# Kernel tuning notes

Hardware: AMD Instinct MI355X
Metric: run time of the kernel (lower is better)

The kernel has to match this reference:

```python
import jax, jax.numpy as jnp
import numpy as np

H = 8
D = 512
DK = D // H  # 64
ALPHA = 0.2  # leaky relu negative slope


def setup_inputs() -> dict:
    key = jax.random.key(0)
    ks = jax.random.split(key, 10)
    B, N = 8, 1024
    query = jax.random.normal(ks[0], (B, N, D), dtype=jnp.float32)
    key_t = jax.random.normal(ks[1], (B, N, D), dtype=jnp.float32)
    value = jax.random.normal(ks[2], (B, N, D), dtype=jnp.float32)
    mask = jax.random.randint(ks[3], (B, N, N), 0, 2, dtype=jnp.int32)
    scale = 0.02
    Wq = jax.random.normal(ks[4], (D, D), dtype=jnp.float32) * scale
    Wk = jax.random.normal(ks[5], (D, D), dtype=jnp.float32) * scale
    Wv = jax.random.normal(ks[6], (D, D), dtype=jnp.float32) * scale
    Wo = jax.random.normal(ks[7], (D, D), dtype=jnp.float32) * scale
    bq = jnp.zeros((D,), jnp.float32)
    bk = jnp.zeros((D,), jnp.float32)
    bv = jnp.zeros((D,), jnp.float32)
    bo = jnp.zeros((D,), jnp.float32)
    # xavier-uniform-like init for the attention vector a: shape (h, 2*d_k)
    limit = float(np.sqrt(6.0 / (H + 2 * DK)))
    a = jax.random.uniform(ks[8], (H, 2 * DK), dtype=jnp.float32, minval=-limit, maxval=limit)
    return {"query": query, "key": key_t, "value": value, "mask": mask,
            "Wq": Wq, "bq": bq, "Wk": Wk, "bk": bk, "Wv": Wv, "bv": bv,
            "Wo": Wo, "bo": bo, "a": a}


def reference(query, key, value, mask, Wq, bq, Wk, bk, Wv, bv, Wo, bo, a):
    B, N, _ = query.shape

    def proj(x, W, b):
        # torch Linear: x @ W.T + b, then split heads -> (B, H, N, DK)
        return (x @ W.T + b).reshape(B, N, H, DK).transpose(0, 2, 1, 3)

    q = proj(query, Wq, bq)
    k = proj(key, Wk, bk)
    v = proj(value, Wv, bv)

    # 'cat' attention: scores[b,h,i,j] = concat(q_i, k_j) . a[h]
    #                = q_i . a[h,:DK] + k_j . a[h,DK:]  (algebraic decomposition,
    #                 avoids the O(N^2 * 2*DK) concat tensor of the torch code)
    sq = jnp.einsum('bhnd,hd->bhn', q, a[:, :DK])
    sk = jnp.einsum('bhnd,hd->bhn', k, a[:, DK:])
    scores = sq[:, :, :, None] + sk[:, :, None, :]  # (B, H, N, N)

    # mask == 0 -> -inf (mask broadcast over heads), applied BEFORE leaky relu
    scores = jnp.where(mask[:, None, :, :] == 0, -jnp.inf, scores)
    # leaky relu (leaky_relu(-inf) == -inf, preserved)
    scores = jnp.where(scores >= 0, scores, ALPHA * scores)

    p = jax.nn.softmax(scores, axis=-1)
    # fully-masked rows produce NaN -> replace with 0 (as in the torch code)
    p = jnp.where(jnp.isnan(p), jnp.zeros_like(p), p)

    x = jnp.einsum('bhnm,bhmd->bhnd', p, v)
    x = x.transpose(0, 2, 1, 3).reshape(B, N, D)
    return x @ Wo.T + bo
```

## Files before the change

### kernel.cpp

```cpp
#include <hip/hip_runtime.h>
#include <hip/hip_bf16.h>
#include <stdint.h>


typedef __attribute__((ext_vector_type(8))) short short8;
typedef __attribute__((ext_vector_type(4))) float f32x4;

#define LB __launch_bounds__(256)

union U8 { unsigned u[4]; short8 s; uint4 v; };
union U2 { unsigned u[2]; uint2 v; };

__device__ __forceinline__ unsigned short f2bf(float f) {
  unsigned int u = __float_as_uint(f);
  u += 0x7fffu + ((u >> 16) & 1u);
  return (unsigned short)(u >> 16);
}

__device__ __forceinline__ unsigned cvt_pk(float a, float b) {
  unsigned r;
  asm("v_cvt_pk_bf16_f32 %0, %1, %2" : "=v"(r) : "v"(a), "v"(b));
  return r;
}

__device__ __forceinline__ void async_cp16(const void* g, void* l) {
  __builtin_amdgcn_global_load_lds(
      (const __attribute__((address_space(1))) unsigned int*)g,
      (__attribute__((address_space(3))) unsigned int*)l, 16, 0, 0);
}

__global__ LB void prep_kernel(const float* __restrict__ Wq, const float* __restrict__ Wk,
                               const float* __restrict__ a, const float* __restrict__ bq,
                               const float* __restrict__ bk,
                               unsigned short* __restrict__ Bfrag, float* __restrict__ qkb,
                               const float* __restrict__ Wv, const float* __restrict__ Wo,
                               unsigned short* __restrict__ wv16,
                               unsigned short* __restrict__ wo16) {
  const int blk = blockIdx.x;
  if (blk < 512) {
    const float* src = blk < 256 ? Wv : Wo;
    unsigned short* dst = blk < 256 ? wv16 : wo16;
    const int idx = ((blk & 255) * 256 + threadIdx.x) * 4;
    const float4 v = *(const float4*)(src + idx);
    U2 pk;
    pk.u[0] = cvt_pk(v.x, v.y);
    pk.u[1] = cvt_pk(v.z, v.w);
    *(uint2*)(dst + idx) = pk.v;
    return;
  }
  const int t = (blk - 512) * 256 + threadIdx.x;
  const int d = t & 511, h = t >> 9;
  float aq = 0.f, ak = 0.f;
#pragma unroll 4
  for (int dk = 0; dk < 64; ++dk) {
    aq += Wq[(size_t)(h * 64 + dk) * 512 + d] * a[h * 128 + dk];
    ak += Wk[(size_t)(h * 64 + dk) * 512 + d] * a[h * 128 + 64 + dk];
  }
  const float L2E = 1.4426950408889634f;
  const int ks = d >> 5, lch = (d >> 3) & 3, tt = d & 7;
  Bfrag[((ks * 64 + (lch << 4) + h) << 3) + tt] = f2bf(aq * L2E);
  Bfrag[((ks * 64 + (lch << 4) + 8 + h) << 3) + tt] = f2bf(ak * L2E);
  if (d == 0) {
    float s1 = 0.f, s2 = 0.f;
    for (int dk = 0; dk < 64; ++dk) {
      s1 += bq[h * 64 + dk] * a[h * 128 + dk];
      s2 += bk[h * 64 + dk] * a[h * 128 + 64 + dk];
    }
    qkb[h] = s1 * L2E;
    qkb[8 + h] = s2 * L2E;
  }
}

__global__ LB void sqsk_kernel(const float* __restrict__ query, const float* __restrict__ key,
                               const unsigned short* __restrict__ Bfrag,
                               const float* __restrict__ qkb,
                               float* __restrict__ sq, float* __restrict__ sk) {
  __shared__ float comb[3 * 64 * 9];
  const int tid = threadIdx.x, wv = tid >> 6, l = tid & 63;
  const int m0 = blockIdx.x * 16;
  const int k0 = wv * 128;
  short8 bf[4];
#pragma unroll
  for (int ks = 0; ks < 4; ++ks)
    bf[ks] = *(const short8*)(Bfrag + (((wv * 4 + ks) * 64 + l) << 3));
  const float* qbase = query + (size_t)(m0 + (l & 15)) * 512 + k0 + ((l >> 4) << 3);
  const float* kbase = key + (size_t)(m0 + (l & 15)) * 512 + k0 + ((l >> 4) << 3);
  f32x4 cq = {}, ck = {};
#pragma unroll
  for (int ks = 0; ks < 4; ++ks) {
    const float4 q0 = *(const float4*)(qbase + ks * 32);
    const float4 q1 = *(const float4*)(qbase + ks * 32 + 4);
    const float4 k0v = *(const float4*)(kbase + ks * 32);
    const float4 k1v = *(const float4*)(kbase + ks * 32 + 4);
    U8 aq, ak;
    aq.u[0] = cvt_pk(q0.x, q0.y); aq.u[1] = cvt_pk(q0.z, q0.w);
    aq.u[2] = cvt_pk(q1.x, q1.y); aq.u[3] = cvt_pk(q1.z, q1.w);
    ak.u[0] = cvt_pk(k0v.x, k0v.y); ak.u[1] = cvt_pk(k0v.z, k0v.w);
    ak.u[2] = cvt_pk(k1v.x, k1v.y); ak.u[3] = cvt_pk(k1v.z, k1v.w);
    cq = __builtin_amdgcn_mfma_f32_16x16x32_bf16(aq.s, bf[ks], cq, 0, 0, 0);
    ck = __builtin_amdgcn_mfma_f32_16x16x32_bf16(ak.s, bf[ks], ck, 0, 0, 0);
  }
  if (wv) {
    float* p = comb + ((wv - 1) * 64 + l) * 9;
#pragma unroll
    for (int r = 0; r < 4; ++r) { p[r] = cq[r]; p[4 + r] = ck[r]; }
  }
  __syncthreads();
  if (wv == 0) {
#pragma unroll
    for (int j = 0; j < 3; ++j) {
      const float* p = comb + (j * 64 + l) * 9;
#pragma unroll
      for (int r = 0; r < 4; ++r) { cq[r] += p[r]; ck[r] += p[4 + r]; }
    }
    const int col = l & 15;
    const int mbase = m0 + ((l >> 4) << 2);
    const int b = mbase >> 10;
    const float bia = qkb[col];
    if (col < 8) {
      float* out = sq + ((size_t)b * 8 + col) * 1024;
#pragma unroll
      for (int r = 0; r < 4; ++r) out[(mbase + r) & 1023] = cq[r] + bia;
    } else {
      float* out = sk + ((size_t)b * 8 + (col - 8)) * 1024;
#pragma unroll
      for (int r = 0; r < 4; ++r) out[(mbase + r) & 1023] = ck[r] + bia;
    }
  }
}

__global__ LB void maskbits_kernel(const int* __restrict__ mask,
                                   unsigned int* __restrict__ bits) {
  const size_t idx = (size_t)blockIdx.x * 256 + threadIdx.x;
  const unsigned long long bl = __ballot(mask[idx] != 0);
  if ((threadIdx.x & 63) == 0) {
    bits[idx >> 5] = (unsigned int)bl;
    bits[(idx >> 5) + 1] = (unsigned int)(bl >> 32);
  }
}

template <int AB16, int BB16, int MODE>
__global__ LB void gemm_bt(const void* __restrict__ Ap,
                           const void* __restrict__ Bwp,
                           const float* __restrict__ bias, void* __restrict__ outp) {
  __shared__ unsigned short As[32 * 32];
  __shared__ unsigned short Bs[128 * 32];
  const int tid = threadIdx.x;
  const int w = tid >> 6, l = tid & 63;
  const int lr = l & 15, lc = l >> 4;
  const int bm = blockIdx.x >> 2, bn = blockIdx.x & 3;
  const int m0 = bm * 32, n0 = bn * 128;
  const int wr = (w & 1) * 16, wc = (w >> 1) * 64;
  const int rch = (lc ^ ((lr >> 1) & 3)) << 3;
  const int crow = l >> 2;
  const int sc = (l & 3) ^ ((l >> 3) & 3);
  const unsigned short* a16 = (const unsigned short*)Ap;
  const unsigned short* b16 = (const unsigned short*)Bwp;
  const float* b32 = (const float*)Bwp;
  const unsigned short* bsrc0 = nullptr; const unsigned short* bsrc1 = nullptr;
  if (BB16) {
    bsrc0 = b16 + (size_t)(n0 + (w << 4) + crow) * 512 + (sc << 3);
    bsrc1 = b16 + (size_t)(n0 + ((w + 4) << 4) + crow) * 512 + (sc << 3);
  }
  const unsigned short* asrc = nullptr;
  if (AB16)
    asrc = a16 + (size_t)(m0 + ((w >> 1) << 4) + crow) * 512 + (sc << 3);

  f32x4 acc[4] = {};
  for (int kt = 0; kt < 16; ++kt) {
    const int k0 = kt * 32;
    if (kt) __syncthreads();
    if (AB16) {
      if (!(w & 1)) async_cp16(asrc + k0, As + ((w >> 1) << 9));
    } else {
      if (tid < 128) {
        const int row = tid >> 2, gr = tid & 3;
        const int sch = (gr ^ ((row >> 1) & 3)) << 3;
        const float4* src = (const float4*)((const float*)Ap + (size_t)(m0 + row) * 512 + k0 + gr * 8);
        const float4 a0 = src[0], a1 = src[1];
        U8 t8;
        t8.u[0] = cvt_pk(a0.x, a0.y); t8.u[1] = cvt_pk(a0.z, a0.w);
        t8.u[2] = cvt_pk(a1.x, a1.y); t8.u[3] = cvt_pk(a1.z, a1.w);
        *(uint4*)(As + row * 32 + sch) = t8.v;
      }
    }
    if (BB16) {
      async_cp16(bsrc0 + k0, Bs + (w << 9));
      async_cp16(bsrc1 + k0, Bs + ((w + 4) << 9));
    } else {
#pragma unroll
      for (int it = 0; it < 2; ++it) {
        const int idx = it * 256 + tid;
        const int row = idx >> 2, gr = idx & 3;
        const int sch = (gr ^ ((row >> 1) & 3)) << 3;
        const float4* src = (const float4*)(b32 + (size_t)(n0 + row) * 512 + k0 + gr * 8);
        const float4 b0 = src[0], b1 = src[1];
        U8 t8;
        t8.u[0] = cvt_pk(b0.x, b0.y); t8.u[1] = cvt_pk(b0.z, b0.w);
        t8.u[2] = cvt_pk(b1.x, b1.y); t8.u[3] = cvt_pk(b1.z, b1.w);
        *(uint4*)(Bs + row * 32 + sch) = t8.v;
      }
    }
    __syncthreads();
    const short8 af = *(const short8*)(As + (wr + lr) * 32 + rch);
#pragma unroll
    for (int j = 0; j < 4; ++j) {
      const short8 bfr = *(const short8*)(Bs + (wc + j * 16 + lr) * 32 + rch);
      acc[j] = __builtin_amdgcn_mfma_f32_16x16x32_bf16(af, bfr, acc[j], 0, 0, 0);
    }
  }
#pragma unroll
  for (int j = 0; j < 4; ++j) {
    const int nn = n0 + wc + j * 16 + lr;
    const float bia = bias[nn];
    const int mm0 = m0 + wr + lc * 4;
    if (MODE == 0) {
      float* out = (float*)outp;
#pragma unroll
      for (int r = 0; r < 4; ++r)
        out[(size_t)(mm0 + r) * 512 + nn] = acc[j][r] + bia;
    } else {
      unsigned short* out = (unsigned short*)outp;
      const int b = mm0 >> 10, t0 = mm0 & 1023;
      const int h = nn >> 6, dk = nn & 63;
      U2 pk;
      pk.u[0] = cvt_pk(acc[j][0] + bia, acc[j][1] + bia);
      pk.u[1] = cvt_pk(acc[j][2] + bia, acc[j][3] + bia);
      *(uint2*)(out + (((size_t)((b * 8 + h) * 64 + dk)) << 10) + t0) = pk.v;
    }
  }
}

__global__ LB void attn_kernel(const float* __restrict__ sq, const float* __restrict__ sk,
                               const unsigned char* __restrict__ mbits,
                               const unsigned short* __restrict__ vt,
                               unsigned short* __restrict__ xb) {
  __shared__ char smem[20480];
  unsigned short* vts = (unsigned short*)smem;
  float* sks = (float*)(smem + 8192);
  char* mks = smem + 12288;
  const int tid = threadIdx.x;
  const int w = tid >> 6, l = tid & 63;
  const int lr = l & 15, lc = l >> 4;
  const int bid = blockIdx.x;
  const int bh = bid >> 4, iblk = bid & 15;
  const int b = bh >> 3, h = bh & 7;
  const int i0b = iblk * 64;
  const float* sqp = sq + (size_t)bh * 1024;
  const float* skp = sk + (size_t)bh * 1024;
  const unsigned short* vtp = vt + ((size_t)bh << 16);
  const unsigned char* mrow = mbits + ((size_t)b << 17);

  async_cp16(skp + (w << 8) + l * 4, sks + (w << 8));
#pragma unroll
  for (int m = 0; m < 2; ++m) {
    const int row = (w << 4) + (m << 3) + (l >> 3);
    const int c = (l & 7) ^ (row & 7);
    async_cp16(mrow + (size_t)(i0b + row) * 128 + (c << 4), mks + (w << 11) + (m << 10));
  }
  const int strow = (w << 4) + (l >> 2);
  const int stc = (l & 3) ^ ((strow >> 1) & 3);
  const unsigned short* srcw = vtp + strow * 1024 + (stc << 3);
  async_cp16(srcw, vts + (w << 9));

  const int rowl = (w << 4) + lr;
  const float sq1 = sqp[i0b + rowl];
  __syncthreads();

  f32x4 acc[4] = {};
  f32x4 accs = {};
  short8 ones;
#pragma unroll
  for (int t = 0; t < 8; ++t) ones[t] = (short)0x3f80;
  const int mrowbase = rowl << 7;
  const int rxorb = (rowl & 7) << 4;
  const int vread = (lc ^ ((lr >> 1) & 3)) << 3;

  int cur = 0;
  for (int jt = 0; jt < 32; ++jt) {
    if (jt < 31) {
      async_cp16(srcw + (jt + 1) * 32, vts + ((cur ^ 1) << 11) + (w << 9));
      asm volatile("s_waitcnt vmcnt(1)" ::: "memory");
    } else {
      asm volatile("s_waitcnt vmcnt(0)" ::: "memory");
    }
    __builtin_amdgcn_sched_barrier(0);
    __builtin_amdgcn_s_barrier();
    const int jb = jt << 5;
    const unsigned int mb = (unsigned char)mks[mrowbase + ((jt * 4 + lc) ^ rxorb)];
    const f32x4 s0 = *(const f32x4*)(sks + jb + (lc << 3));
    const f32x4 s1 = *(const f32x4*)(sks + jb + (lc << 3) + 4);
    float e[8];
#pragma unroll
    for (int t = 0; t < 8; ++t) {
      float s = sq1 + (t < 4 ? s0[t] : s1[t - 4]);
      s = fmaxf(s, 0.2f * s);
      const float ex = __builtin_amdgcn_exp2f(s);
      e[t] = (mb & (1u << t)) ? ex : 0.0f;
    }
    U8 pa;
    pa.u[0] = cvt_pk(e[0], e[1]); pa.u[1] = cvt_pk(e[2], e[3]);
    pa.u[2] = cvt_pk(e[4], e[5]); pa.u[3] = cvt_pk(e[6], e[7]);
    const unsigned short* vb_base = vts + (cur << 11) + vread;
#pragma unroll
    for (int c = 0; c < 4; ++c) {
      const short8 bv = *(const short8*)(vb_base + ((c << 4) + lr) * 32);
      acc[c] = __builtin_amdgcn_mfma_f32_16x16x32_bf16(pa.s, bv, acc[c], 0, 0, 0);
    }
    accs = __builtin_amdgcn_mfma_f32_16x16x32_bf16(pa.s, ones, accs, 0, 0, 0);
    if (jt < 31) __builtin_amdgcn_s_barrier();
    cur ^= 1;
  }

#pragma unroll
  for (int r = 0; r < 4; ++r) {
    const float s = accs[r];
    const float inv = s > 0.0f ? 1.0f / s : 0.0f;
    const int i = i0b + (w << 4) + lc * 4 + r;
#pragma unroll
    for (int c = 0; c < 4; ++c)
      xb[(((size_t)(b * 1024 + i)) << 9) + h * 64 + c * 16 + lr] =
          f2bf(acc[c][r] * inv);
  }
}

extern "C" void kernel_launch(void* const* d_in, const int* in_sizes, int n_in,
                              void* d_out, int out_size, void* d_ws, size_t ws_size,
                              hipStream_t stream) {
  const float* query = (const float*)d_in[0];
  const float* key   = (const float*)d_in[1];
  const float* value = (const float*)d_in[2];
  const int*   mask  = (const int*)d_in[3];
  const float* Wq = (const float*)d_in[4];
  const float* bq = (const float*)d_in[5];
  const float* Wk = (const float*)d_in[6];
  const float* bk = (const float*)d_in[7];
  const float* Wv = (const float*)d_in[8];
  const float* bv = (const float*)d_in[9];
  const float* Wo = (const float*)d_in[10];
  const float* bo = (const float*)d_in[11];
  const float* a  = (const float*)d_in[12];

  char* oc = (char*)d_out;
  unsigned short* vt = (unsigned short*)(oc + 0);
  unsigned int* mbits = (unsigned int*)(oc + 8388608);
  float* sqv = (float*)(oc + 9437184);
  float* skv = (float*)(oc + 9699328);
  unsigned short* Bfrag = (unsigned short*)(oc + 9961472);
  float* qkb = (float*)(oc + 9977856);
  unsigned short* wv16 = (unsigned short*)(oc + 10485760);
  unsigned short* wo16f = (unsigned short*)(oc + 11010048);
  unsigned short* xb = (unsigned short*)d_ws;

  const bool roomy = ws_size >= 8912896;
  unsigned short* wo16 = roomy ? (unsigned short*)((char*)d_ws + 8388608) : wo16f;

  prep_kernel<<<528, 256, 0, stream>>>(Wq, Wk, a, bq, bk, Bfrag, qkb, Wv, Wo, wv16, wo16);
  sqsk_kernel<<<512, 256, 0, stream>>>(query, key, Bfrag, qkb, sqv, skv);
  maskbits_kernel<<<32768, 256, 0, stream>>>(mask, mbits);
  gemm_bt<0, 1, 1><<<1024, 256, 0, stream>>>((const void*)value, (const void*)wv16, bv, (void*)vt);
  attn_kernel<<<1024, 256, 0, stream>>>(sqv, skv, (const unsigned char*)mbits, vt, xb);
  if (roomy)
    gemm_bt<1, 1, 0><<<1024, 256, 0, stream>>>((const void*)xb, (const void*)wo16, bo, d_out);
  else
    gemm_bt<1, 0, 0><<<1024, 256, 0, stream>>>((const void*)xb, (const void*)Wo, bo, d_out);
}
```

Baseline: 94.44 us.

## Fuse mask/value conversion into prep kernel and double-buffer GEMM and attention loads

Merges the maskbits pass and a new fp32-to-bf16 conversion of the value tensor into the prep kernel, which removes one launch. The V projection GEMM then reads bf16 input through async loads. The GEMM gets a double-buffered async-copy pipeline with s_setprio around the MFMAs. The attention kernel now stages two 32-column V tiles per barrier pair, halving the barrier count at the cost of more LDS. Precomputing bf16 value adds a write and re-read of an 8MB buffer, and it shares the workspace with xb.

```diff
diff --git a/kernel.cpp b/kernel.cpp
--- a/kernel.cpp
+++ b/kernel.cpp
@@ -29,18 +29,38 @@
       (__attribute__((address_space(3))) unsigned int*)l, 16, 0, 0);
 }
 
-__global__ LB void prep_kernel(const float* __restrict__ Wq, const float* __restrict__ Wk,
+__global__ LB void prep_kernel(const int* __restrict__ mask, unsigned int* __restrict__ bits,
+                               const float* __restrict__ value, unsigned short* __restrict__ vb,
+                               const float* __restrict__ Wv, const float* __restrict__ Wo,
+                               unsigned short* __restrict__ wv16, unsigned short* __restrict__ wo16,
+                               const float* __restrict__ Wq, const float* __restrict__ Wk,
                                const float* __restrict__ a, const float* __restrict__ bq,
                                const float* __restrict__ bk,
-                               unsigned short* __restrict__ Bfrag, float* __restrict__ qkb,
-                               const float* __restrict__ Wv, const float* __restrict__ Wo,
-                               unsigned short* __restrict__ wv16,
-                               unsigned short* __restrict__ wo16) {
+                               unsigned short* __restrict__ Bfrag, float* __restrict__ qkb) {
   const int blk = blockIdx.x;
-  if (blk < 512) {
-    const float* src = blk < 256 ? Wv : Wo;
-    unsigned short* dst = blk < 256 ? wv16 : wo16;
-    const int idx = ((blk & 255) * 256 + threadIdx.x) * 4;
+  if (blk < 32768) {
+    const size_t idx = (size_t)blk * 256 + threadIdx.x;
+    const unsigned long long bl = __ballot(mask[idx] != 0);
+    if ((threadIdx.x & 63) == 0) {
+      bits[idx >> 5] = (unsigned int)bl;
+      bits[(idx >> 5) + 1] = (unsigned int)(bl >> 32);
+    }
+    return;
+  }
+  if (blk < 36864) {
+    const int idx = ((blk - 32768) * 256 + threadIdx.x) * 4;
+    const float4 v = *(const float4*)(value + idx);
+    U2 pk;
+    pk.u[0] = cvt_pk(v.x, v.y);
+    pk.u[1] = cvt_pk(v.z, v.w);
+    *(uint2*)(vb + idx) = pk.v;
+    return;
+  }
+  if (blk < 37376) {
+    const int wblk = blk - 36864;
+    const float* src = wblk < 256 ? Wv : Wo;
+    unsigned short* dst = wblk < 256 ? wv16 : wo16;
+    const int idx = ((wblk & 255) * 256 + threadIdx.x) * 4;
     const float4 v = *(const float4*)(src + idx);
     U2 pk;
     pk.u[0] = cvt_pk(v.x, v.y);
@@ -48,7 +68,7 @@
     *(uint2*)(dst + idx) = pk.v;
     return;
   }
-  const int t = (blk - 512) * 256 + threadIdx.x;
+  const int t = (blk - 37376) * 256 + threadIdx.x;
   const int d = t & 511, h = t >> 9;
   float aq = 0.f, ak = 0.f;
 #pragma unroll 4
@@ -129,22 +149,12 @@
   }
 }
 
-__global__ LB void maskbits_kernel(const int* __restrict__ mask,
-                                   unsigned int* __restrict__ bits) {
-  const size_t idx = (size_t)blockIdx.x * 256 + threadIdx.x;
-  const unsigned long long bl = __ballot(mask[idx] != 0);
-  if ((threadIdx.x & 63) == 0) {
-    bits[idx >> 5] = (unsigned int)bl;
-    bits[(idx >> 5) + 1] = (unsigned int)(bl >> 32);
-  }
-}
-
-template <int AB16, int BB16, int MODE>
-__global__ LB void gemm_bt(const void* __restrict__ Ap,
+template <int BB16, int MODE>
+__global__ LB void gemm_bt(const unsigned short* __restrict__ A,
                            const void* __restrict__ Bwp,
                            const float* __restrict__ bias, void* __restrict__ outp) {
-  __shared__ unsigned short As[32 * 32];
-  __shared__ unsigned short Bs[128 * 32];
+  __shared__ unsigned short As[2][32 * 32];
+  __shared__ unsigned short Bs[2][128 * 32];
   const int tid = threadIdx.x;
   const int w = tid >> 6, l = tid & 63;
   const int lr = l & 15, lc = l >> 4;
@@ -152,42 +162,50 @@
   const int m0 = bm * 32, n0 = bn * 128;
   const int wr = (w & 1) * 16, wc = (w >> 1) * 64;
   const int rch = (lc ^ ((lr >> 1) & 3)) << 3;
+  const int arow = (w << 3) + (l >> 2);
+  const int asc = (l & 3) ^ ((arow >> 1) & 3);
+  const unsigned short* asrc = A + (size_t)(m0 + arow) * 512 + (asc << 3);
   const int crow = l >> 2;
-  const int sc = (l & 3) ^ ((l >> 3) & 3);
-  const unsigned short* a16 = (const unsigned short*)Ap;
   const unsigned short* b16 = (const unsigned short*)Bwp;
   const float* b32 = (const float*)Bwp;
-  const unsigned short* bsrc0 = nullptr; const unsigned short* bsrc1 = nullptr;
+  const int brow0 = (w << 4) + crow, brow1 = ((w + 4) << 4) + crow;
+  const unsigned short* bsrc0 = b16 + (size_t)(n0 + brow0) * 512 + (((l & 3) ^ ((brow0 >> 1) & 3)) << 3);
+  const unsigned short* bsrc1 = b16 + (size_t)(n0 + brow1) * 512 + (((l & 3) ^ ((brow1 >> 1) & 3)) << 3);
+
+  f32x4 acc[4] = {};
   if (BB16) {
-    bsrc0 = b16 + (size_t)(n0 + (w << 4) + crow) * 512 + (sc << 3);
-    bsrc1 = b16 + (size_t)(n0 + ((w + 4) << 4) + crow) * 512 + (sc << 3);
-  }
-  const unsigned short* asrc = nullptr;
-  if (AB16)
-    asrc = a16 + (size_t)(m0 + ((w >> 1) << 4) + crow) * 512 + (sc << 3);
-
-  f32x4 acc[4] = {};
-  for (int kt = 0; kt < 16; ++kt) {
-    const int k0 = kt * 32;
-    if (kt) __syncthreads();
-    if (AB16) {
-      if (!(w & 1)) async_cp16(asrc + k0, As + ((w >> 1) << 9));
-    } else {
-      if (tid < 128) {
-        const int row = tid >> 2, gr = tid & 3;
-        const int sch = (gr ^ ((row >> 1) & 3)) << 3;
-        const float4* src = (const float4*)((const float*)Ap + (size_t)(m0 + row) * 512 + k0 + gr * 8);
-        const float4 a0 = src[0], a1 = src[1];
-        U8 t8;
-        t8.u[0] = cvt_pk(a0.x, a0.y); t8.u[1] = cvt_pk(a0.z, a0.w);
-        t8.u[2] = cvt_pk(a1.x, a1.y); t8.u[3] = cvt_pk(a1.z, a1.w);
-        *(uint4*)(As + row * 32 + sch) = t8.v;
-      }
-    }
-    if (BB16) {
-      async_cp16(bsrc0 + k0, Bs + (w << 9));
-      async_cp16(bsrc1 + k0, Bs + ((w + 4) << 9));
-    } else {
+    if (l < 32) async_cp16(asrc, As[0] + (w << 8));
+    async_cp16(bsrc0, Bs[0] + (w << 9));
+    async_cp16(bsrc1, Bs[0] + ((w + 4) << 9));
+    int buf = 0;
+    for (int kt = 0; kt < 16; ++kt) {
+      if (kt < 15) {
+        const int k1 = (kt + 1) * 32;
+        if (l < 32) async_cp16(asrc + k1, As[buf ^ 1] + (w << 8));
+        async_cp16(bsrc0 + k1, Bs[buf ^ 1] + (w << 9));
+        async_cp16(bsrc1 + k1, Bs[buf ^ 1] + ((w + 4) << 9));
+        asm volatile("s_waitcnt vmcnt(3)" ::: "memory");
+      } else {
+        asm volatile("s_waitcnt vmcnt(0)" ::: "memory");
+      }
+      __builtin_amdgcn_sched_barrier(0);
+      __builtin_amdgcn_s_barrier();
+      const short8 af = *(const short8*)(As[buf] + (wr + lr) * 32 + rch);
+      __builtin_amdgcn_s_setprio(1);
+#pragma unroll
+      for (int j = 0; j < 4; ++j) {
+        const short8 bfr = *(const short8*)(Bs[buf] + (wc + j * 16 + lr) * 32 + rch);
+        acc[j] = __builtin_amdgcn_mfma_f32_16x16x32_bf16(af, bfr, acc[j], 0, 0, 0);
+      }
+      __builtin_amdgcn_s_setprio(0);
+      if (kt < 15) __builtin_amdgcn_s_barrier();
+      buf ^= 1;
+    }
+  } else {
+    for (int kt = 0; kt < 16; ++kt) {
+      const int k0 = kt * 32;
+      if (kt) __syncthreads();
+      if (l < 32) async_cp16(asrc + k0, As[0] + (w << 8));
 #pragma unroll
       for (int it = 0; it < 2; ++it) {
         const int idx = it * 256 + tid;
@@ -198,15 +216,15 @@
         U8 t8;
         t8.u[0] = cvt_pk(b0.x, b0.y); t8.u[1] = cvt_pk(b0.z, b0.w);
         t8.u[2] = cvt_pk(b1.x, b1.y); t8.u[3] = cvt_pk(b1.z, b1.w);
-        *(uint4*)(Bs + row * 32 + sch) = t8.v;
-      }
-    }
-    __syncthreads();
-    const short8 af = *(const short8*)(As + (wr + lr) * 32 + rch);
-#pragma unroll
-    for (int j = 0; j < 4; ++j) {
-      const short8 bfr = *(const short8*)(Bs + (wc + j * 16 + lr) * 32 + rch);
-      acc[j] = __builtin_amdgcn_mfma_f32_16x16x32_bf16(af, bfr, acc[j], 0, 0, 0);
+        *(uint4*)(Bs[0] + row * 32 + sch) = t8.v;
+      }
+      __syncthreads();
+      const short8 af = *(const short8*)(As[0] + (wr + lr) * 32 + rch);
+#pragma unroll
+      for (int j = 0; j < 4; ++j) {
+        const short8 bfr = *(const short8*)(Bs[0] + (wc + j * 16 + lr) * 32 + rch);
+        acc[j] = __builtin_amdgcn_mfma_f32_16x16x32_bf16(af, bfr, acc[j], 0, 0, 0);
+      }
     }
   }
 #pragma unroll
@@ -235,10 +253,10 @@
                                const unsigned char* __restrict__ mbits,
                                const unsigned short* __restrict__ vt,
                                unsigned short* __restrict__ xb) {
-  __shared__ char smem[20480];
+  __shared__ char smem[28672];
   unsigned short* vts = (unsigned short*)smem;
-  float* sks = (float*)(smem + 8192);
-  char* mks = smem + 12288;
+  float* sks = (float*)(smem + 16384);
+  char* mks = smem + 20480;
   const int tid = threadIdx.x;
   const int w = tid >> 6, l = tid & 63;
   const int lr = l & 15, lc = l >> 4;
@@ -262,6 +280,7 @@
   const int stc = (l & 3) ^ ((strow >> 1) & 3);
   const unsigned short* srcw = vtp + strow * 1024 + (stc << 3);
   async_cp16(srcw, vts + (w << 9));
+  async_cp16(srcw + 32, vts + 2048 + (w << 9));
 
   const int rowl = (w << 4) + lr;
   const float sq1 = sqp[i0b + rowl];
@@ -276,40 +295,48 @@
   const int rxorb = (rowl & 7) << 4;
   const int vread = (lc ^ ((lr >> 1) & 3)) << 3;
 
-  int cur = 0;
-  for (int jt = 0; jt < 32; ++jt) {
-    if (jt < 31) {
-      async_cp16(srcw + (jt + 1) * 32, vts + ((cur ^ 1) << 11) + (w << 9));
-      asm volatile("s_waitcnt vmcnt(1)" ::: "memory");
+  int bufp = 0;
+  for (int it = 0; it < 16; ++it) {
+    if (it < 15) {
+      const int sl = (it + 1) << 1;
+      unsigned short* dst = vts + ((bufp ^ 1) << 12) + (w << 9);
+      async_cp16(srcw + sl * 32, dst);
+      async_cp16(srcw + sl * 32 + 32, dst + 2048);
+      asm volatile("s_waitcnt vmcnt(2)" ::: "memory");
     } else {
       asm volatile("s_waitcnt vmcnt(0)" ::: "memory");
     }
     __builtin_amdgcn_sched_barrier(0);
     __builtin_amdgcn_s_barrier();
-    const int jb = jt << 5;
-    const unsigned int mb = (unsigned char)mks[mrowbase + ((jt * 4 + lc) ^ rxorb)];
-    const f32x4 s0 = *(const f32x4*)(sks + jb + (lc << 3));
-    const f32x4 s1 = *(const f32x4*)(sks + jb + (lc << 3) + 4);
-    float e[8];
-#pragma unroll
-    for (int t = 0; t < 8; ++t) {
-      float s = sq1 + (t < 4 ? s0[t] : s1[t - 4]);
-      s = fmaxf(s, 0.2f * s);
-      const float ex = __builtin_amdgcn_exp2f(s);
-      e[t] = (mb & (1u << t)) ? ex : 0.0f;
-    }
-    U8 pa;
-    pa.u[0] = cvt_pk(e[0], e[1]); pa.u[1] = cvt_pk(e[2], e[3]);
-    pa.u[2] = cvt_pk(e[4], e[5]); pa.u[3] = cvt_pk(e[6], e[7]);
-    const unsigned short* vb_base = vts + (cur << 11) + vread;
-#pragma unroll
-    for (int c = 0; c < 4; ++c) {
-      const short8 bv = *(const short8*)(vb_base + ((c << 4) + lr) * 32);
-      acc[c] = __builtin_amdgcn_mfma_f32_16x16x32_bf16(pa.s, bv, acc[c], 0, 0, 0);
-    }
-    accs = __builtin_amdgcn_mfma_f32_16x16x32_bf16(pa.s, ones, accs, 0, 0, 0);
-    if (jt < 31) __builtin_amdgcn_s_barrier();
-    cur ^= 1;
+#pragma unroll
+    for (int sub = 0; sub < 2; ++sub) {
+      const int jb = (it << 6) + (sub << 5);
+      const unsigned int mb = (unsigned char)mks[mrowbase + (((jb >> 3) + lc) ^ rxorb)];
+      const f32x4 s0 = *(const f32x4*)(sks + jb + (lc << 3));
+      const f32x4 s1 = *(const f32x4*)(sks + jb + (lc << 3) + 4);
+      float e[8];
+#pragma unroll
+      for (int t = 0; t < 8; ++t) {
+        float s = sq1 + (t < 4 ? s0[t] : s1[t - 4]);
+        s = fmaxf(s, 0.2f * s);
+        const float ex = __builtin_amdgcn_exp2f(s);
+        e[t] = (mb & (1u << t)) ? ex : 0.0f;
+      }
+      U8 pa;
+      pa.u[0] = cvt_pk(e[0], e[1]); pa.u[1] = cvt_pk(e[2], e[3]);
+      pa.u[2] = cvt_pk(e[4], e[5]); pa.u[3] = cvt_pk(e[6], e[7]);
+      const unsigned short* vb_base = vts + (bufp << 12) + (sub << 11) + vread;
+      __builtin_amdgcn_s_setprio(1);
+#pragma unroll
+      for (int c = 0; c < 4; ++c) {
+        const short8 bv = *(const short8*)(vb_base + ((c << 4) + lr) * 32);
+        acc[c] = __builtin_amdgcn_mfma_f32_16x16x32_bf16(pa.s, bv, acc[c], 0, 0, 0);
+      }
+      accs = __builtin_amdgcn_mfma_f32_16x16x32_bf16(pa.s, ones, accs, 0, 0, 0);
+      __builtin_amdgcn_s_setprio(0);
+    }
+    if (it < 15) __builtin_amdgcn_s_barrier();
+    bufp ^= 1;
   }
 
 #pragma unroll
@@ -350,18 +377,19 @@
   float* qkb = (float*)(oc + 9977856);
   unsigned short* wv16 = (unsigned short*)(oc + 10485760);
   unsigned short* wo16f = (unsigned short*)(oc + 11010048);
+  unsigned short* vb = (unsigned short*)d_ws;
   unsigned short* xb = (unsigned short*)d_ws;
 
   const bool roomy = ws_size >= 8912896;
   unsigned short* wo16 = roomy ? (unsigned short*)((char*)d_ws + 8388608) : wo16f;
 
-  prep_kernel<<<528, 256, 0, stream>>>(Wq, Wk, a, bq, bk, Bfrag, qkb, Wv, Wo, wv16, wo16);
+  prep_kernel<<<37392, 256, 0, stream>>>(mask, mbits, value, vb, Wv, Wo, wv16, wo16,
+                                         Wq, Wk, a, bq, bk, Bfrag, qkb);
   sqsk_kernel<<<512, 256, 0, stream>>>(query, key, Bfrag, qkb, sqv, skv);
-  maskbits_kernel<<<32768, 256, 0, stream>>>(mask, mbits);
-  gemm_bt<0, 1, 1><<<1024, 256, 0, stream>>>((const void*)value, (const void*)wv16, bv, (void*)vt);
+  gemm_bt<1, 1><<<1024, 256, 0, stream>>>(vb, (const void*)wv16, bv, (void*)vt);
   attn_kernel<<<1024, 256, 0, stream>>>(sqv, skv, (const unsigned char*)mbits, vt, xb);
   if (roomy)
-    gemm_bt<1, 1, 0><<<1024, 256, 0, stream>>>((const void*)xb, (const void*)wo16, bo, d_out);
+    gemm_bt<1, 0><<<1024, 256, 0, stream>>>(xb, (const void*)wo16, bo, d_out);
   else
-    gemm_bt<1, 0, 0><<<1024, 256, 0, stream>>>((const void*)xb, (const void*)Wo, bo, d_out);
-}
+    gemm_bt<0, 0><<<1024, 256, 0, stream>>>(xb, (const void*)Wo, bo, d_out);
+}
```

Measured after the change: 90.43 us. 4.3% less time.
